# Kernel tuning notes

Measured on AMD Instinct MI355X. Metric: run time of the kernel, lower is better.

Reference implementation:

```python
import jax, jax.numpy as jnp
import numpy as np

NB_OBJ = 5
DIM_BODY = 10
DIM_OBJ = 15
N_PERM = NB_OBJ * (NB_OBJ - 1)  # 20
LOG_STD_MIN, LOG_STD_MAX = -20.0, 2.0


def _linear_init(key, fan_in, fan_out):
    k1, k2 = jax.random.split(key)
    lim = 1.0 / np.sqrt(fan_in)
    W = jax.random.uniform(k1, (fan_in, fan_out), minval=-lim, maxval=lim, dtype=jnp.float32)
    b = jax.random.uniform(k2, (fan_out,), minval=-lim, maxval=lim, dtype=jnp.float32)
    return W, b


def setup_inputs() -> dict:
    key = jax.random.key(0)
    ks = jax.random.split(key, 12)
    B = 16384
    # graph structure (constants)
    perms = [(i, j) for i in range(NB_OBJ) for j in range(NB_OBJ) if i != j]
    src = jnp.array([p[0] for p in perms], dtype=jnp.int32)   # [E]
    dst = jnp.array([p[1] for p in perms], dtype=jnp.int32)   # [E]
    inc = jnp.array([[k for k, p in enumerate(perms) if p[1] == i] for i in range(NB_OBJ)], dtype=jnp.int32)  # [O,4]
    pred = jnp.arange(2 * N_PERM, dtype=jnp.int32).reshape(N_PERM, 2)  # predicate ids per edge
    # parameters
    mp_W1, mp_b1 = _linear_init(ks[0], 8, 256)
    mp_W2, mp_b2 = _linear_init(ks[1], 256, 128)
    ea_W, ea_b = _linear_init(ks[2], 128, 1)
    phi_W1, phi_b1 = _linear_init(ks[3], 153, 256)
    phi_W2, phi_b2 = _linear_init(ks[4], 256, 128)
    sa_W, sa_b = _linear_init(ks[5], 128, 1)
    rho_W1, rho_b1 = _linear_init(ks[6], 128, 256)
    mean_W, mean_b = _linear_init(ks[7], 256, 4)
    ls_W, ls_b = _linear_init(ks[8], 256, 4)
    obs = jax.random.normal(ks[9], (B, DIM_BODY + NB_OBJ * DIM_OBJ), dtype=jnp.float32)
    ag = jax.random.normal(ks[10], (B, 2 * N_PERM), dtype=jnp.float32)
    g = jax.random.normal(ks[11], (B, 2 * N_PERM), dtype=jnp.float32)
    return dict(obs=obs, ag=ag, g=g,
                mp_W1=mp_W1, mp_b1=mp_b1, mp_W2=mp_W2, mp_b2=mp_b2,
                ea_W=ea_W, ea_b=ea_b,
                phi_W1=phi_W1, phi_b1=phi_b1, phi_W2=phi_W2, phi_b2=phi_b2,
                sa_W=sa_W, sa_b=sa_b,
                rho_W1=rho_W1, rho_b1=rho_b1,
                mean_W=mean_W, mean_b=mean_b, ls_W=ls_W, ls_b=ls_b,
                src=src, dst=dst, inc=inc, pred=pred)


def reference(obs, ag, g,
              mp_W1, mp_b1, mp_W2, mp_b2,
              ea_W, ea_b,
              phi_W1, phi_b1, phi_W2, phi_b2,
              sa_W, sa_b,
              rho_W1, rho_b1,
              mean_W, mean_b, ls_W, ls_b,
              src, dst, inc, pred):
    B = obs.shape[0]
    body = obs[:, :DIM_BODY]                                    # [B,10]
    objs = obs[:, DIM_BODY:].reshape(B, NB_OBJ, DIM_OBJ)        # [B,O,15]
    delta_g = g - ag                                            # [B,40]
    # --- message passing over edges (vectorized gather + cat) ---
    e_pred = delta_g[:, pred]                                   # [B,E,2]
    e_src = objs[:, src, :3]                                    # [B,E,3]
    e_dst = objs[:, dst, :3]                                    # [B,E,3]
    inp_mp = jnp.concatenate([e_pred, e_src, e_dst], axis=-1)   # [B,E,8]
    h = jax.nn.relu(inp_mp @ mp_W1 + mp_b1)
    mp_out = jax.nn.relu(h @ mp_W2 + mp_b2)                     # [B,E,128]
    # --- edge self-attention pooling per object over incoming edges ---
    per_obj = mp_out[:, inc]                                    # [B,O,K,128]
    w = jax.nn.softmax(per_obj @ ea_W + ea_b, axis=2)           # softmax over incoming set
    edge_feat = jnp.sum(w * per_obj, axis=2)                    # [B,O,128]
    # --- deep-set phi over objects ---
    body_rep = jnp.broadcast_to(body[:, None, :], (B, NB_OBJ, DIM_BODY))
    inp = jnp.concatenate([body_rep, objs, edge_feat], axis=-1)  # [B,O,153]
    ph = jax.nn.relu(inp @ phi_W1 + phi_b1)
    phi_out = jax.nn.relu(ph @ phi_W2 + phi_b2)                  # [B,O,128]
    aw = jax.nn.softmax(phi_out @ sa_W + sa_b, axis=1)           # softmax over objects
    pooled = jnp.sum(aw * phi_out, axis=1)                       # [B,128]
    # --- rho actor head ---
    r = jax.nn.relu(pooled @ rho_W1 + rho_b1)
    mean = r @ mean_W + mean_b
    logstd = jnp.clip(r @ ls_W + ls_b, LOG_STD_MIN, LOG_STD_MAX)
    return mean, logstd
```

## Files before the change

kernel.cpp:

```cpp
#include <hip/hip_runtime.h>
#include <cstdint>
#include <cstddef>

typedef unsigned short u16;
typedef unsigned int u32;
typedef __attribute__((ext_vector_type(8))) short bf16x8;
typedef __attribute__((ext_vector_type(4))) float f32x4;

#define MFMA16(A, B, C) __builtin_amdgcn_mfma_f32_16x16x32_bf16((A), (B), (C), 0, 0, 0)

__device__ __forceinline__ u16 bf16_rne(float x) {
    u32 u = __float_as_uint(x);
    u += 0x7fffu + ((u >> 16) & 1u);
    return (u16)(u >> 16);
}
__device__ __forceinline__ float bf2f(u16 h) { return __uint_as_float((u32)h << 16); }
__device__ __forceinline__ u16 bf16_lo(float x, u16 hi) { return bf16_rne(x - bf2f(hi)); }
__device__ __forceinline__ float blo(u32 u) { return __uint_as_float(u << 16); }
__device__ __forceinline__ float bhi(u32 u) { return __uint_as_float(u & 0xffff0000u); }
__device__ __forceinline__ u32 cvt_pk(float a, float b) {
    u32 r;
    asm("v_cvt_pk_bf16_f32 %0, %1, %2" : "=v"(r) : "v"(a), "v"(b));
    return r;
}

__device__ __forceinline__ void PK_body(int tid,
    const float* __restrict__ mpW1, const float* __restrict__ mpW2,
    const float* __restrict__ phW1, const float* __restrict__ phW2,
    const float* __restrict__ rhoW,
    u16* __restrict__ Bp1e, u16* __restrict__ Bp2e,
    u16* __restrict__ BpC1, u16* __restrict__ BpC2, u16* __restrict__ BpR)
{
    if (tid < 8192) {
        int t = tid >> 9, r = tid & 511;
        int l = r >> 3, i = r & 7, g = l >> 4, l15 = l & 15;
        float w = mpW1[i * 256 + 16 * t + l15];
        u16 h = bf16_rne(w);
        Bp1e[tid] = (g < 2) ? h : bf16_lo(w, h);
    } else if (tid < 73728) {
        int f = tid - 8192;
        int b5 = f >> 9, r = f & 511;
        int l = r >> 3, i = r & 7, g = l >> 4, l15 = l & 15;
        int s = b5 & 1, cn = b5 >> 1, c = cn >> 3, n = cn & 7;
        int kk = 32 * c + 8 * g + i;
        float w = mpW2[kk * 128 + 16 * n + l15];
        u16 h = bf16_rne(w);
        Bp2e[f] = s ? bf16_lo(w, h) : h;
    } else if (tid < 155648) {
        int f = tid - 73728;
        int b5 = f >> 9, r = f & 511;
        int l = r >> 3, i = r & 7, g = l >> 4, l15 = l & 15;
        int t = b5 & 15, cs = b5 >> 4, s = cs & 1, c = cs >> 1;
        int kk = 32 * c + 8 * g + i;
        int kp = kk < 25 ? kk : (kk < 32 ? -1 : kk - 7);
        float w = (kp < 0) ? 0.0f : phW1[kp * 256 + 16 * t + l15];
        u16 h = bf16_rne(w);
        BpC1[f] = s ? bf16_lo(w, h) : h;
    } else if (tid < 221184) {
        int f = tid - 155648;
        int b5 = f >> 9, r = f & 511;
        int l = r >> 3, i = r & 7, g = l >> 4, l15 = l & 15;
        int s = b5 & 1, cn = b5 >> 1, c = cn >> 3, n = cn & 7;
        int kk = 32 * c + 8 * g + i;
        float w = phW2[kk * 128 + 16 * n + l15];
        u16 h = bf16_rne(w);
        BpC2[f] = s ? bf16_lo(w, h) : h;
    } else {
        int f = tid - 221184;
        int b5 = f >> 9, r = f & 511;
        int l = r >> 3, i = r & 7, g = l >> 4, l15 = l & 15;
        int s = b5 & 1, ct = b5 >> 1, c = ct >> 4, t = ct & 15;
        int kk = 32 * c + 8 * g + i;
        float w = rhoW[kk * 256 + 16 * t + l15];
        u16 h = bf16_rne(w);
        BpR[f] = s ? bf16_lo(w, h) : h;
    }
}

__device__ __forceinline__ void P1_body(int row,
    const float* __restrict__ obs, const float* __restrict__ ag, const float* __restrict__ g,
    const int* __restrict__ src, const int* __restrict__ dst, const int* __restrict__ pred,
    u16* __restrict__ Ein)
{
    int b = row / 20, p = row - b * 20;
    float inp[8];
    int i0 = pred[2 * p], i1 = pred[2 * p + 1];
    const float* gb = g + (size_t)b * 40;
    const float* ab = ag + (size_t)b * 40;
    inp[0] = gb[i0] - ab[i0];
    inp[1] = gb[i1] - ab[i1];
    int so = src[p], dd = dst[p];
    const float* ob = obs + (size_t)b * 85 + 10;
    inp[2] = ob[so * 15 + 0]; inp[3] = ob[so * 15 + 1]; inp[4] = ob[so * 15 + 2];
    inp[5] = ob[dd * 15 + 0]; inp[6] = ob[dd * 15 + 1]; inp[7] = ob[dd * 15 + 2];

    u32 wh[4], wl[4];
    #pragma unroll
    for (int k = 0; k < 4; ++k) {
        u16 h0 = bf16_rne(inp[2 * k]), h1 = bf16_rne(inp[2 * k + 1]);
        u16 l0 = bf16_lo(inp[2 * k], h0), l1 = bf16_lo(inp[2 * k + 1], h1);
        wh[k] = (u32)h0 | ((u32)h1 << 16);
        wl[k] = (u32)l0 | ((u32)l1 << 16);
    }
    uint4* d4 = (uint4*)(Ein + (size_t)row * 16);
    d4[0] = make_uint4(wh[0], wh[1], wh[2], wh[3]);
    d4[1] = make_uint4(wl[0], wl[1], wl[2], wl[3]);
}

__global__ __launch_bounds__(256) void PREP(
    const float* __restrict__ mpW1, const float* __restrict__ mpW2,
    const float* __restrict__ phW1, const float* __restrict__ phW2,
    const float* __restrict__ rhoW,
    u16* __restrict__ Bp1e, u16* __restrict__ Bp2e,
    u16* __restrict__ BpC1, u16* __restrict__ BpC2, u16* __restrict__ BpR,
    const float* __restrict__ obs, const float* __restrict__ ag, const float* __restrict__ g,
    const int* __restrict__ src, const int* __restrict__ dst, const int* __restrict__ pred,
    u16* __restrict__ Ein,
    const float* __restrict__ meanW, const float* __restrict__ lsW,
    float* __restrict__ headWpk)
{
    int bid = blockIdx.x;
    if (bid < 1120) {
        PK_body(bid * 256 + threadIdx.x, mpW1, mpW2, phW1, phW2, rhoW, Bp1e, Bp2e, BpC1, BpC2, BpR);
    } else if (bid < 2400) {
        P1_body((bid - 1120) * 256 + threadIdx.x, obs, ag, g, src, dst, pred, Ein);
    } else {
        int idx = threadIdx.x;
        #pragma unroll
        for (int r = 0; r < 8; ++r) {
            int f = r * 256 + idx;
            int k = f >> 3, q = f & 7;
            headWpk[f] = (q < 4) ? meanW[k * 4 + q] : lsW[k * 4 + (q - 4)];
        }
    }
}

__global__ __launch_bounds__(512) void GA(
    const u16* __restrict__ Ein, const u16* __restrict__ Bp1, const u16* __restrict__ Bp2,
    const float* __restrict__ b1, const float* __restrict__ b2,
    const float* __restrict__ eaW, const float* __restrict__ eab,
    const int* __restrict__ inc, const float* __restrict__ obs,
    u16* __restrict__ Nin)
{
    __shared__ u16 hb[3][16 * 256];
    __shared__ u16 mpb[80 * 128];
    __shared__ float spart[8][80];
    __shared__ float wbuf[80];
    __shared__ int rowb[80];
    __shared__ int incL[20];

    const int tid = threadIdx.x;
    const int w = tid >> 6, lane = tid & 63;
    const int l15 = lane & 15, gq = lane >> 4;
    const int rowbase = blockIdx.x * 80;
    char* hbc = (char*)hb;
    char* mpc = (char*)mpb;

    if (tid < 20) incL[tid] = inc[tid];

    bf16x8 B1[2];
    float4 b1v[2];
    #pragma unroll
    for (int t = 0; t < 2; ++t) {
        B1[t] = *(const bf16x8*)(Bp1 + (size_t)(2 * w + t) * 512 + lane * 8);
        b1v[t] = *(const float4*)(b1 + 16 * (2 * w + t) + 4 * gq);
    }
    bf16x8 B2[8];
    #pragma unroll
    for (int c = 0; c < 8; ++c)
        B2[c] = *(const bf16x8*)(Bp2 + (size_t)((c * 8 + w) * 2) * 512 + lane * 8);
    const float4 b2v = *(const float4*)(b2 + 16 * w + 4 * gq);
    const float4 eav = *(const float4*)(eaW + 16 * w + 4 * gq);

    auto ldX = [&](int m) {
        return *(const bf16x8*)(Ein + (size_t)(rowbase + m * 16 + l15) * 16 + 8 * (gq & 1));
    };
    auto stage1 = [&](int buf, const bf16x8& X) {
        #pragma unroll
        for (int t = 0; t < 2; ++t) {
            f32x4 acc = {b1v[t].x, b1v[t].y, b1v[t].z, b1v[t].w};
            acc = MFMA16(B1[t], X, acc);
            u32 p0 = cvt_pk(fmaxf(acc[0], 0.f), fmaxf(acc[1], 0.f));
            u32 p1 = cvt_pk(fmaxf(acc[2], 0.f), fmaxf(acc[3], 0.f));
            int colu = 16 * (2 * w + t) + 4 * gq;
            int byte = buf * 8192 + ((l15 * 512 + colu * 2) ^ ((l15 & 7) << 4));
            *(uint2*)(hbc + byte) = make_uint2(p0, p1);
        }
    };
    auto stage2 = [&](int m, int buf) {
        f32x4 accA = {b2v.x, b2v.y, b2v.z, b2v.w};
        f32x4 accB = {0.f, 0.f, 0.f, 0.f};
        #pragma unroll
        for (int c = 0; c < 4; ++c) {
            int byteA = buf * 8192 + ((l15 * 512 + (2 * c) * 64 + gq * 16) ^ ((l15 & 7) << 4));
            int byteB = buf * 8192 + ((l15 * 512 + (2 * c + 1) * 64 + gq * 16) ^ ((l15 & 7) << 4));
            const bf16x8 HA = *(const bf16x8*)(hbc + byteA);
            const bf16x8 HB = *(const bf16x8*)(hbc + byteB);
            accA = MFMA16(B2[2 * c], HA, accA);
            accB = MFMA16(B2[2 * c + 1], HB, accB);
        }
        float v0 = fmaxf(accA[0] + accB[0], 0.f), v1 = fmaxf(accA[1] + accB[1], 0.f);
        float v2 = fmaxf(accA[2] + accB[2], 0.f), v3 = fmaxf(accA[3] + accB[3], 0.f);
        float ep = v0 * eav.x + v1 * eav.y + v2 * eav.z + v3 * eav.w;
        ep += __shfl_xor(ep, 16, 64);
        ep += __shfl_xor(ep, 32, 64);
        if (gq == 0) spart[w][m * 16 + l15] = ep;
        u32 p0 = cvt_pk(v0, v1), p1 = cvt_pk(v2, v3);
        int r = m * 16 + l15;
        int byte2 = (r * 256 + (16 * w + 4 * gq) * 2) ^ ((r & 15) << 4);
        *(uint2*)(mpc + byte2) = make_uint2(p0, p1);
    };

    {
        bf16x8 X0 = ldX(0);
        bf16x8 X1 = ldX(1);
        stage1(0, X0);
        stage1(1, X1);
    }
    __syncthreads();
    {
        bf16x8 X2 = ldX(2);
        stage2(0, 0);
        stage2(1, 1);
        stage1(2, X2);
    }
    __syncthreads();
    {
        bf16x8 X3 = ldX(3);
        bf16x8 X4 = ldX(4);
        stage2(2, 2);
        stage1(0, X3);
        stage1(1, X4);
    }
    __syncthreads();
    stage2(3, 0);
    stage2(4, 1);
    __syncthreads();

    if (tid < 20) {
        int bl = tid / 5, o = tid - bl * 5;
        const float e0 = eab[0];
        int rr[4]; float ee[4];
        #pragma unroll
        for (int i = 0; i < 4; ++i) {
            rr[i] = bl * 20 + incL[o * 4 + i];
            float e = e0;
            #pragma unroll
            for (int ww = 0; ww < 8; ++ww) e += spart[ww][rr[i]];
            ee[i] = e;
        }
        float mx = fmaxf(fmaxf(ee[0], ee[1]), fmaxf(ee[2], ee[3]));
        float ex[4]; float den = 0.f;
        #pragma unroll
        for (int i = 0; i < 4; ++i) { ex[i] = __expf(ee[i] - mx); den += ex[i]; }
        float inv = 1.0f / den;
        #pragma unroll
        for (int i = 0; i < 4; ++i) {
            wbuf[tid * 4 + i] = ex[i] * inv;
            rowb[tid * 4 + i] = rr[i];
        }
    } else if (tid >= 320 && tid < 480) {
        int t2 = tid - 320;
        int p = t2 >> 3, q = t2 & 7;
        int bl = p / 5, o = p - bl * 5;
        const float* body = obs + (size_t)(blockIdx.x * 4 + bl) * 85;
        const float* op = body + 10 + o * 15;
        float v[4];
        #pragma unroll
        for (int jj = 0; jj < 4; ++jj) {
            int col = 4 * q + jj;
            v[jj] = (col < 10) ? body[col] : (col < 25) ? op[col - 10] : 0.0f;
        }
        int grow = blockIdx.x * 20 + p;
        *(uint2*)(Nin + (size_t)grow * 160 + 4 * q) =
            make_uint2(cvt_pk(v[0], v[1]), cvt_pk(v[2], v[3]));
    }
    __syncthreads();

    if (tid < 320) {
        int p = tid >> 4, cb = tid & 15;
        float acc[8] = {0, 0, 0, 0, 0, 0, 0, 0};
        #pragma unroll
        for (int i = 0; i < 4; ++i) {
            int r = rowb[p * 4 + i];
            float wi = wbuf[p * 4 + i];
            int byte = (r * 256 + cb * 16) ^ ((r & 15) << 4);
            uint4 v = *(const uint4*)(mpc + byte);
            acc[0] = fmaf(wi, blo(v.x), acc[0]);
            acc[1] = fmaf(wi, bhi(v.x), acc[1]);
            acc[2] = fmaf(wi, blo(v.y), acc[2]);
            acc[3] = fmaf(wi, bhi(v.y), acc[3]);
            acc[4] = fmaf(wi, blo(v.z), acc[4]);
            acc[5] = fmaf(wi, bhi(v.z), acc[5]);
            acc[6] = fmaf(wi, blo(v.w), acc[6]);
            acc[7] = fmaf(wi, bhi(v.w), acc[7]);
        }
        uint4 ov;
        ov.x = cvt_pk(acc[0], acc[1]);
        ov.y = cvt_pk(acc[2], acc[3]);
        ov.z = cvt_pk(acc[4], acc[5]);
        ov.w = cvt_pk(acc[6], acc[7]);
        int grow = blockIdx.x * 20 + p;
        *(uint4*)(Nin + (size_t)grow * 160 + 32 + cb * 8) = ov;
    }
}

__global__ __launch_bounds__(512) void GB(
    const u16* __restrict__ Nin, const u16* __restrict__ BpC1, const u16* __restrict__ BpC2,
    const u16* __restrict__ BpR,
    const float* __restrict__ b1, const float* __restrict__ b2,
    const float* __restrict__ saW, const float* __restrict__ sab,
    const float* __restrict__ rhob, const float* __restrict__ headWpk,
    const float* __restrict__ meanb, const float* __restrict__ lsb,
    float* __restrict__ outp)
{
    __shared__ u16 hb[4][16 * 256];
    __shared__ u16 phibuf[80 * 132];
    __shared__ float spart[8][80];
    __shared__ float awb[80];

    const int tid = threadIdx.x;
    const int w = tid >> 6, lane = tid & 63;
    const int l15 = lane & 15, gq = lane >> 4;
    const int rowbase = blockIdx.x * 80;
    char* hbc = (char*)hb;
    float* rbuf = (float*)phibuf;
    float* hpart = (float*)spart;
    u32* poolw = (u32*)hb;

    bf16x8 BC[5][2];
    float4 b1v[2];
    #pragma unroll
    for (int t = 0; t < 2; ++t) b1v[t] = *(const float4*)(b1 + 16 * (2 * w + t) + 4 * gq);
    #pragma unroll
    for (int c = 0; c < 5; ++c)
        #pragma unroll
        for (int t = 0; t < 2; ++t)
            BC[c][t] = *(const bf16x8*)(BpC1 + (size_t)((c * 2) * 16 + 2 * w + t) * 512 + lane * 8);
    bf16x8 B2[8];
    #pragma unroll
    for (int c = 0; c < 8; ++c)
        B2[c] = *(const bf16x8*)(BpC2 + (size_t)((c * 8 + w) * 2) * 512 + lane * 8);
    const float4 b2v = *(const float4*)(b2 + 16 * w + 4 * gq);
    const float4 sav = *(const float4*)(saW + 16 * w + 4 * gq);

    auto loadX = [&](int m, bf16x8* X) {
        #pragma unroll
        for (int c = 0; c < 5; ++c)
            X[c] = *(const bf16x8*)(Nin + (size_t)(rowbase + m * 16 + l15) * 160 + 32 * c + 8 * gq);
    };
    auto stage1 = [&](int buf, const bf16x8* X) {
        f32x4 a0 = {b1v[0].x, b1v[0].y, b1v[0].z, b1v[0].w};
        f32x4 a1 = {b1v[1].x, b1v[1].y, b1v[1].z, b1v[1].w};
        #pragma unroll
        for (int c = 0; c < 5; ++c) {
            a0 = MFMA16(BC[c][0], X[c], a0);
            a1 = MFMA16(BC[c][1], X[c], a1);
        }
        #pragma unroll
        for (int t = 0; t < 2; ++t) {
            const f32x4& a = t ? a1 : a0;
            u32 p0 = cvt_pk(fmaxf(a[0], 0.f), fmaxf(a[1], 0.f));
            u32 p1 = cvt_pk(fmaxf(a[2], 0.f), fmaxf(a[3], 0.f));
            int colu = 16 * (2 * w + t) + 4 * gq;
            int byte = buf * 8192 + ((l15 * 512 + colu * 2) ^ ((l15 & 7) << 4));
            *(uint2*)(hbc + byte) = make_uint2(p0, p1);
        }
    };
    auto stage2 = [&](int m, int buf) {
        f32x4 accA = {b2v.x, b2v.y, b2v.z, b2v.w};
        f32x4 accB = {0.f, 0.f, 0.f, 0.f};
        #pragma unroll
        for (int c = 0; c < 4; ++c) {
            int byteA = buf * 8192 + ((l15 * 512 + (2 * c) * 64 + gq * 16) ^ ((l15 & 7) << 4));
            int byteB = buf * 8192 + ((l15 * 512 + (2 * c + 1) * 64 + gq * 16) ^ ((l15 & 7) << 4));
            const bf16x8 HA = *(const bf16x8*)(hbc + byteA);
            const bf16x8 HB = *(const bf16x8*)(hbc + byteB);
            accA = MFMA16(B2[2 * c], HA, accA);
            accB = MFMA16(B2[2 * c + 1], HB, accB);
        }
        float v0 = fmaxf(accA[0] + accB[0], 0.f), v1 = fmaxf(accA[1] + accB[1], 0.f);
        float v2 = fmaxf(accA[2] + accB[2], 0.f), v3 = fmaxf(accA[3] + accB[3], 0.f);
        int r = m * 16 + l15;
        *(uint2*)((char*)phibuf + r * 264 + (16 * w + 4 * gq) * 2) =
            make_uint2(cvt_pk(v0, v1), cvt_pk(v2, v3));
        float sp = v0 * sav.x + v1 * sav.y + v2 * sav.z + v3 * sav.w;
        sp += __shfl_xor(sp, 16, 64);
        sp += __shfl_xor(sp, 32, 64);
        if (gq == 0) spart[w][r] = sp;
    };

    {
        bf16x8 X0[5], X1[5];
        loadX(0, X0);
        loadX(1, X1);
        stage1(0, X0);
        stage1(1, X1);
    }
    __syncthreads();
    {
        bf16x8 X2[5], X3[5];
        loadX(2, X2);
        loadX(3, X3);
        stage2(0, 0);
        stage2(1, 1);
        stage1(2, X2);
        stage1(3, X3);
    }
    __syncthreads();
    {
        bf16x8 X4[5];
        loadX(4, X4);
        stage2(2, 2);
        stage2(3, 3);
        stage1(0, X4);
    }
    __syncthreads();
    stage2(4, 0);
    __syncthreads();

    if (tid < 16) {
        const float s0c = sab[0];
        float ss[5];
        #pragma unroll
        for (int o = 0; o < 5; ++o) {
            float s = s0c;
            #pragma unroll
            for (int ww = 0; ww < 8; ++ww) s += spart[ww][tid * 5 + o];
            ss[o] = s;
        }
        float mx = fmaxf(fmaxf(fmaxf(ss[0], ss[1]), fmaxf(ss[2], ss[3])), ss[4]);
        float ex[5]; float den = 0.f;
        #pragma unroll
        for (int o = 0; o < 5; ++o) { ex[o] = __expf(ss[o] - mx); den += ex[o]; }
        float inv = 1.0f / den;
        #pragma unroll
        for (int o = 0; o < 5; ++o) awb[tid * 5 + o] = ex[o] * inv;
    }
    __syncthreads();

    #pragma unroll
    for (int rep = 0; rep < 2; ++rep) {
        int idx = rep * 512 + tid;
        int b = idx >> 6, cw = idx & 63;
        float p0 = 0.f, p1 = 0.f;
        #pragma unroll
        for (int o = 0; o < 5; ++o) {
            u32 v = *(const u32*)((const char*)phibuf + (size_t)(b * 5 + o) * 264 + cw * 4);
            float a = awb[b * 5 + o];
            p0 = fmaf(a, blo(v), p0);
            p1 = fmaf(a, bhi(v), p1);
        }
        u16 h0 = bf16_rne(p0); u16 l0 = bf16_lo(p0, h0);
        u16 h1 = bf16_rne(p1); u16 l1 = bf16_lo(p1, h1);
        *(uint2*)(poolw + b * 132 + 2 * cw) =
            make_uint2((u32)h0 | ((u32)l0 << 16), (u32)h1 | ((u32)l1 << 16));
    }
    __syncthreads();

    {
        float4 rb0 = *(const float4*)(rhob + 16 * (2 * w + 0) + 4 * gq);
        float4 rb1 = *(const float4*)(rhob + 16 * (2 * w + 1) + 4 * gq);
        f32x4 acc0 = {rb0.x, rb0.y, rb0.z, rb0.w};
        f32x4 acc1 = {rb1.x, rb1.y, rb1.z, rb1.w};
        #pragma unroll
        for (int c = 0; c < 4; ++c) {
            uint4 q0 = *(const uint4*)(poolw + l15 * 132 + 32 * c + 8 * gq);
            uint4 q1 = *(const uint4*)(poolw + l15 * 132 + 32 * c + 8 * gq + 4);
            u32 ws[8] = {q0.x, q0.y, q0.z, q0.w, q1.x, q1.y, q1.z, q1.w};
            bf16x8 Ph, Pl;
            #pragma unroll
            for (int i = 0; i < 8; ++i) {
                Ph[i] = (short)(ws[i] & 0xffffu);
                Pl[i] = (short)(ws[i] >> 16);
            }
            #pragma unroll
            for (int t = 0; t < 2; ++t) {
                bf16x8 Bh = *(const bf16x8*)(BpR + (size_t)((c * 16 + 2 * w + t) * 2 + 0) * 512 + lane * 8);
                f32x4& a = t ? acc1 : acc0;
                a = MFMA16(Bh, Ph, a);
                a = MFMA16(Bh, Pl, a);
            }
        }
        #pragma unroll
        for (int t = 0; t < 2; ++t) {
            const f32x4& a = t ? acc1 : acc0;
            float4 v;
            v.x = fmaxf(a[0], 0.f); v.y = fmaxf(a[1], 0.f);
            v.z = fmaxf(a[2], 0.f); v.w = fmaxf(a[3], 0.f);
            *(float4*)(rbuf + l15 * 260 + 16 * (2 * w + t) + 4 * gq) = v;
        }
    }
    __syncthreads();

    {
        int s = tid >> 7, p = tid & 127;
        int b = p >> 3, q = p & 7;
        const float* rrow = rbuf + b * 260 + s * 64;
        const float* wcol = headWpk + s * 64 * 8 + q;
        float acc = 0.f;
        #pragma unroll 8
        for (int k = 0; k < 64; ++k)
            acc = fmaf(rrow[k], wcol[k * 8], acc);
        hpart[s * 128 + p] = acc;
    }
    __syncthreads();
    if (tid < 128) {
        int b = tid >> 3, q = tid & 7;
        float a = hpart[tid] + hpart[128 + tid] + hpart[256 + tid] + hpart[384 + tid];
        int bg = blockIdx.x * 16 + b;
        if (q < 4) {
            outp[(size_t)bg * 4 + q] = a + meanb[q];
        } else {
            float l = a + lsb[q - 4];
            outp[65536 + (size_t)bg * 4 + (q - 4)] = fminf(fmaxf(l, -20.0f), 2.0f);
        }
    }
}

extern "C" void kernel_launch(void* const* d_in, const int* in_sizes, int n_in,
                              void* d_out, int out_size, void* d_ws, size_t ws_size,
                              hipStream_t stream)
{
    const float* obs   = (const float*)d_in[0];
    const float* ag    = (const float*)d_in[1];
    const float* g     = (const float*)d_in[2];
    const float* mpW1  = (const float*)d_in[3];
    const float* mpb1  = (const float*)d_in[4];
    const float* mpW2  = (const float*)d_in[5];
    const float* mpb2  = (const float*)d_in[6];
    const float* eaW   = (const float*)d_in[7];
    const float* eab   = (const float*)d_in[8];
    const float* phW1  = (const float*)d_in[9];
    const float* phb1  = (const float*)d_in[10];
    const float* phW2  = (const float*)d_in[11];
    const float* phb2  = (const float*)d_in[12];
    const float* saW   = (const float*)d_in[13];
    const float* sab   = (const float*)d_in[14];
    const float* rhoW  = (const float*)d_in[15];
    const float* rhob  = (const float*)d_in[16];
    const float* meanW = (const float*)d_in[17];
    const float* meanb = (const float*)d_in[18];
    const float* lsW   = (const float*)d_in[19];
    const float* lsb   = (const float*)d_in[20];
    const int*   src   = (const int*)d_in[21];
    const int*   dst   = (const int*)d_in[22];
    const int*   inc   = (const int*)d_in[23];
    const int*   pred  = (const int*)d_in[24];

    char* ws = (char*)d_ws;
    u16* Ein  = (u16*)(ws + 0);
    u16* Nin  = (u16*)(ws + 10485760ull);
    u16* Bp1e = (u16*)(ws + 36700160ull);
    u16* Bp2e = (u16*)(ws + 36716544ull);
    u16* BpC1 = (u16*)(ws + 36847616ull);
    u16* BpC2 = (u16*)(ws + 37011456ull);
    u16* BpR  = (u16*)(ws + 37142528ull);
    float* headWpk = (float*)(ws + 37273600ull);

    hipLaunchKernelGGL(PREP, dim3(2401), dim3(256), 0, stream,
                       mpW1, mpW2, phW1, phW2, rhoW, Bp1e, Bp2e, BpC1, BpC2, BpR,
                       obs, ag, g, src, dst, pred, Ein, meanW, lsW, headWpk);
    hipLaunchKernelGGL(GA, dim3(4096), dim3(512), 0, stream,
                       Ein, Bp1e, Bp2e, mpb1, mpb2, eaW, eab, inc, obs, Nin);
    hipLaunchKernelGGL(GB, dim3(1024), dim3(512), 0, stream,
                       Nin, BpC1, BpC2, BpR, phb1, phb2, saW, sab, rhob,
                       headWpk, meanb, lsb, (float*)d_out);
}
```

Baseline: 98.45 us.

## Fuse edge and node kernels into one kernel, keeping node inputs in LDS

Merges the edge message-passing kernel (GA) and the node/deep-set kernel (GB) into a single kernel GF with 1024 blocks. Each block loops over four 80-edge groups to build its 80 node input rows directly in shared memory, so the Nin global buffer round trip and one launch go away. In exchange the grid is 4x smaller, and the larger LDS footprint (~76KB) and heavier per-block work may reduce occupancy and latency hiding.

Result: slower. 105.3 us (+6.9%).

```diff
diff --git a/kernel.cpp b/kernel.cpp
--- a/kernel.cpp
+++ b/kernel.cpp
@@ -135,385 +135,378 @@
     }
 }
 
-__global__ __launch_bounds__(512) void GA(
+__global__ __launch_bounds__(512) void GF(
     const u16* __restrict__ Ein, const u16* __restrict__ Bp1, const u16* __restrict__ Bp2,
-    const float* __restrict__ b1, const float* __restrict__ b2,
+    const float* __restrict__ eb1, const float* __restrict__ eb2,
     const float* __restrict__ eaW, const float* __restrict__ eab,
     const int* __restrict__ inc, const float* __restrict__ obs,
-    u16* __restrict__ Nin)
-{
-    __shared__ u16 hb[3][16 * 256];
-    __shared__ u16 mpb[80 * 128];
-    __shared__ float spart[8][80];
-    __shared__ float wbuf[80];
-    __shared__ int rowb[80];
-    __shared__ int incL[20];
-
-    const int tid = threadIdx.x;
-    const int w = tid >> 6, lane = tid & 63;
-    const int l15 = lane & 15, gq = lane >> 4;
-    const int rowbase = blockIdx.x * 80;
-    char* hbc = (char*)hb;
-    char* mpc = (char*)mpb;
-
-    if (tid < 20) incL[tid] = inc[tid];
-
-    bf16x8 B1[2];
-    float4 b1v[2];
-    #pragma unroll
-    for (int t = 0; t < 2; ++t) {
-        B1[t] = *(const bf16x8*)(Bp1 + (size_t)(2 * w + t) * 512 + lane * 8);
-        b1v[t] = *(const float4*)(b1 + 16 * (2 * w + t) + 4 * gq);
-    }
-    bf16x8 B2[8];
-    #pragma unroll
-    for (int c = 0; c < 8; ++c)
-        B2[c] = *(const bf16x8*)(Bp2 + (size_t)((c * 8 + w) * 2) * 512 + lane * 8);
-    const float4 b2v = *(const float4*)(b2 + 16 * w + 4 * gq);
-    const float4 eav = *(const float4*)(eaW + 16 * w + 4 * gq);
-
-    auto ldX = [&](int m) {
-        return *(const bf16x8*)(Ein + (size_t)(rowbase + m * 16 + l15) * 16 + 8 * (gq & 1));
-    };
-    auto stage1 = [&](int buf, const bf16x8& X) {
-        #pragma unroll
-        for (int t = 0; t < 2; ++t) {
-            f32x4 acc = {b1v[t].x, b1v[t].y, b1v[t].z, b1v[t].w};
-            acc = MFMA16(B1[t], X, acc);
-            u32 p0 = cvt_pk(fmaxf(acc[0], 0.f), fmaxf(acc[1], 0.f));
-            u32 p1 = cvt_pk(fmaxf(acc[2], 0.f), fmaxf(acc[3], 0.f));
-            int colu = 16 * (2 * w + t) + 4 * gq;
-            int byte = buf * 8192 + ((l15 * 512 + colu * 2) ^ ((l15 & 7) << 4));
-            *(uint2*)(hbc + byte) = make_uint2(p0, p1);
-        }
-    };
-    auto stage2 = [&](int m, int buf) {
-        f32x4 accA = {b2v.x, b2v.y, b2v.z, b2v.w};
-        f32x4 accB = {0.f, 0.f, 0.f, 0.f};
-        #pragma unroll
-        for (int c = 0; c < 4; ++c) {
-            int byteA = buf * 8192 + ((l15 * 512 + (2 * c) * 64 + gq * 16) ^ ((l15 & 7) << 4));
-            int byteB = buf * 8192 + ((l15 * 512 + (2 * c + 1) * 64 + gq * 16) ^ ((l15 & 7) << 4));
-            const bf16x8 HA = *(const bf16x8*)(hbc + byteA);
-            const bf16x8 HB = *(const bf16x8*)(hbc + byteB);
-            accA = MFMA16(B2[2 * c], HA, accA);
-            accB = MFMA16(B2[2 * c + 1], HB, accB);
-        }
-        float v0 = fmaxf(accA[0] + accB[0], 0.f), v1 = fmaxf(accA[1] + accB[1], 0.f);
-        float v2 = fmaxf(accA[2] + accB[2], 0.f), v3 = fmaxf(accA[3] + accB[3], 0.f);
-        float ep = v0 * eav.x + v1 * eav.y + v2 * eav.z + v3 * eav.w;
-        ep += __shfl_xor(ep, 16, 64);
-        ep += __shfl_xor(ep, 32, 64);
-        if (gq == 0) spart[w][m * 16 + l15] = ep;
-        u32 p0 = cvt_pk(v0, v1), p1 = cvt_pk(v2, v3);
-        int r = m * 16 + l15;
-        int byte2 = (r * 256 + (16 * w + 4 * gq) * 2) ^ ((r & 15) << 4);
-        *(uint2*)(mpc + byte2) = make_uint2(p0, p1);
-    };
-
-    {
-        bf16x8 X0 = ldX(0);
-        bf16x8 X1 = ldX(1);
-        stage1(0, X0);
-        stage1(1, X1);
-    }
-    __syncthreads();
-    {
-        bf16x8 X2 = ldX(2);
-        stage2(0, 0);
-        stage2(1, 1);
-        stage1(2, X2);
-    }
-    __syncthreads();
-    {
-        bf16x8 X3 = ldX(3);
-        bf16x8 X4 = ldX(4);
-        stage2(2, 2);
-        stage1(0, X3);
-        stage1(1, X4);
-    }
-    __syncthreads();
-    stage2(3, 0);
-    stage2(4, 1);
-    __syncthreads();
-
-    if (tid < 20) {
-        int bl = tid / 5, o = tid - bl * 5;
-        const float e0 = eab[0];
-        int rr[4]; float ee[4];
-        #pragma unroll
-        for (int i = 0; i < 4; ++i) {
-            rr[i] = bl * 20 + incL[o * 4 + i];
-            float e = e0;
-            #pragma unroll
-            for (int ww = 0; ww < 8; ++ww) e += spart[ww][rr[i]];
-            ee[i] = e;
-        }
-        float mx = fmaxf(fmaxf(ee[0], ee[1]), fmaxf(ee[2], ee[3]));
-        float ex[4]; float den = 0.f;
-        #pragma unroll
-        for (int i = 0; i < 4; ++i) { ex[i] = __expf(ee[i] - mx); den += ex[i]; }
-        float inv = 1.0f / den;
-        #pragma unroll
-        for (int i = 0; i < 4; ++i) {
-            wbuf[tid * 4 + i] = ex[i] * inv;
-            rowb[tid * 4 + i] = rr[i];
-        }
-    } else if (tid >= 320 && tid < 480) {
-        int t2 = tid - 320;
-        int p = t2 >> 3, q = t2 & 7;
-        int bl = p / 5, o = p - bl * 5;
-        const float* body = obs + (size_t)(blockIdx.x * 4 + bl) * 85;
-        const float* op = body + 10 + o * 15;
-        float v[4];
-        #pragma unroll
-        for (int jj = 0; jj < 4; ++jj) {
-            int col = 4 * q + jj;
-            v[jj] = (col < 10) ? body[col] : (col < 25) ? op[col - 10] : 0.0f;
-        }
-        int grow = blockIdx.x * 20 + p;
-        *(uint2*)(Nin + (size_t)grow * 160 + 4 * q) =
-            make_uint2(cvt_pk(v[0], v[1]), cvt_pk(v[2], v[3]));
-    }
-    __syncthreads();
-
-    if (tid < 320) {
-        int p = tid >> 4, cb = tid & 15;
-        float acc[8] = {0, 0, 0, 0, 0, 0, 0, 0};
-        #pragma unroll
-        for (int i = 0; i < 4; ++i) {
-            int r = rowb[p * 4 + i];
-            float wi = wbuf[p * 4 + i];
-            int byte = (r * 256 + cb * 16) ^ ((r & 15) << 4);
-            uint4 v = *(const uint4*)(mpc + byte);
-            acc[0] = fmaf(wi, blo(v.x), acc[0]);
-            acc[1] = fmaf(wi, bhi(v.x), acc[1]);
-            acc[2] = fmaf(wi, blo(v.y), acc[2]);
-            acc[3] = fmaf(wi, bhi(v.y), acc[3]);
-            acc[4] = fmaf(wi, blo(v.z), acc[4]);
-            acc[5] = fmaf(wi, bhi(v.z), acc[5]);
-            acc[6] = fmaf(wi, blo(v.w), acc[6]);
-            acc[7] = fmaf(wi, bhi(v.w), acc[7]);
-        }
-        uint4 ov;
-        ov.x = cvt_pk(acc[0], acc[1]);
-        ov.y = cvt_pk(acc[2], acc[3]);
-        ov.z = cvt_pk(acc[4], acc[5]);
-        ov.w = cvt_pk(acc[6], acc[7]);
-        int grow = blockIdx.x * 20 + p;
-        *(uint4*)(Nin + (size_t)grow * 160 + 32 + cb * 8) = ov;
-    }
-}
-
-__global__ __launch_bounds__(512) void GB(
-    const u16* __restrict__ Nin, const u16* __restrict__ BpC1, const u16* __restrict__ BpC2,
-    const u16* __restrict__ BpR,
-    const float* __restrict__ b1, const float* __restrict__ b2,
+    const u16* __restrict__ BpC1, const u16* __restrict__ BpC2, const u16* __restrict__ BpR,
+    const float* __restrict__ nb1, const float* __restrict__ nb2,
     const float* __restrict__ saW, const float* __restrict__ sab,
     const float* __restrict__ rhob, const float* __restrict__ headWpk,
     const float* __restrict__ meanb, const float* __restrict__ lsb,
     float* __restrict__ outp)
 {
-    __shared__ u16 hb[4][16 * 256];
-    __shared__ u16 phibuf[80 * 132];
-    __shared__ float spart[8][80];
-    __shared__ float awb[80];
-
+    __shared__ __align__(16) char S[76176];
     const int tid = threadIdx.x;
     const int w = tid >> 6, lane = tid & 63;
     const int l15 = lane & 15, gq = lane >> 4;
-    const int rowbase = blockIdx.x * 80;
-    char* hbc = (char*)hb;
-    float* rbuf = (float*)phibuf;
-    float* hpart = (float*)spart;
-    u32* poolw = (u32*)hb;
-
-    bf16x8 BC[5][2];
-    float4 b1v[2];
-    #pragma unroll
-    for (int t = 0; t < 2; ++t) b1v[t] = *(const float4*)(b1 + 16 * (2 * w + t) + 4 * gq);
-    #pragma unroll
-    for (int c = 0; c < 5; ++c)
-        #pragma unroll
-        for (int t = 0; t < 2; ++t)
-            BC[c][t] = *(const bf16x8*)(BpC1 + (size_t)((c * 2) * 16 + 2 * w + t) * 512 + lane * 8);
-    bf16x8 B2[8];
-    #pragma unroll
-    for (int c = 0; c < 8; ++c)
-        B2[c] = *(const bf16x8*)(BpC2 + (size_t)((c * 8 + w) * 2) * 512 + lane * 8);
-    const float4 b2v = *(const float4*)(b2 + 16 * w + 4 * gq);
-    const float4 sav = *(const float4*)(saW + 16 * w + 4 * gq);
-
-    auto loadX = [&](int m, bf16x8* X) {
+    char* hbc = S;
+    char* mpc = S + 24576;
+    char* ninc = S + 45696;
+    float* spart = (float*)(S + 72576);
+    float* wbuf = (float*)(S + 75136);
+    float* awb  = (float*)(S + 75456);
+    int*   rowb = (int*)(S + 75776);
+    int*   incL = (int*)(S + 76096);
+
+    if (tid < 20) incL[tid] = inc[tid];
+
+    {
+        bf16x8 B1[2];
+        float4 b1v[2];
+        #pragma unroll
+        for (int t = 0; t < 2; ++t) {
+            B1[t] = *(const bf16x8*)(Bp1 + (size_t)(2 * w + t) * 512 + lane * 8);
+            b1v[t] = *(const float4*)(eb1 + 16 * (2 * w + t) + 4 * gq);
+        }
+        bf16x8 B2[8];
+        #pragma unroll
+        for (int c = 0; c < 8; ++c)
+            B2[c] = *(const bf16x8*)(Bp2 + (size_t)((c * 8 + w) * 2) * 512 + lane * 8);
+        const float4 b2v = *(const float4*)(eb2 + 16 * w + 4 * gq);
+        const float4 eav = *(const float4*)(eaW + 16 * w + 4 * gq);
+
+        auto stage1e = [&](int buf, const bf16x8& X) {
+            #pragma unroll
+            for (int t = 0; t < 2; ++t) {
+                f32x4 acc = {b1v[t].x, b1v[t].y, b1v[t].z, b1v[t].w};
+                acc = MFMA16(B1[t], X, acc);
+                u32 p0 = cvt_pk(fmaxf(acc[0], 0.f), fmaxf(acc[1], 0.f));
+                u32 p1 = cvt_pk(fmaxf(acc[2], 0.f), fmaxf(acc[3], 0.f));
+                int colu = 16 * (2 * w + t) + 4 * gq;
+                int byte = buf * 8192 + ((l15 * 512 + colu * 2) ^ ((l15 & 7) << 4));
+                *(uint2*)(hbc + byte) = make_uint2(p0, p1);
+            }
+        };
+        auto stage2e = [&](int m, int buf) {
+            f32x4 accA = {b2v.x, b2v.y, b2v.z, b2v.w};
+            f32x4 accB = {0.f, 0.f, 0.f, 0.f};
+            #pragma unroll
+            for (int c = 0; c < 4; ++c) {
+                int byteA = buf * 8192 + ((l15 * 512 + (2 * c) * 64 + gq * 16) ^ ((l15 & 7) << 4));
+                int byteB = buf * 8192 + ((l15 * 512 + (2 * c + 1) * 64 + gq * 16) ^ ((l15 & 7) << 4));
+                const bf16x8 HA = *(const bf16x8*)(hbc + byteA);
+                const bf16x8 HB = *(const bf16x8*)(hbc + byteB);
+                accA = MFMA16(B2[2 * c], HA, accA);
+                accB = MFMA16(B2[2 * c + 1], HB, accB);
+            }
+            float v0 = fmaxf(accA[0] + accB[0], 0.f), v1 = fmaxf(accA[1] + accB[1], 0.f);
+            float v2 = fmaxf(accA[2] + accB[2], 0.f), v3 = fmaxf(accA[3] + accB[3], 0.f);
+            float ep = v0 * eav.x + v1 * eav.y + v2 * eav.z + v3 * eav.w;
+            ep += __shfl_xor(ep, 16, 64);
+            ep += __shfl_xor(ep, 32, 64);
+            if (gq == 0) spart[w * 80 + m * 16 + l15] = ep;
+            u32 p0 = cvt_pk(v0, v1), p1 = cvt_pk(v2, v3);
+            int r = m * 16 + l15;
+            int byte2 = (r * 256 + (16 * w + 4 * gq) * 2) ^ ((r & 15) << 4);
+            *(uint2*)(mpc + byte2) = make_uint2(p0, p1);
+        };
+
+        #pragma unroll 1
+        for (int g = 0; g < 4; ++g) {
+            const int rowbaseE = blockIdx.x * 320 + g * 80;
+            auto ldX = [&](int m) {
+                return *(const bf16x8*)(Ein + (size_t)(rowbaseE + m * 16 + l15) * 16 + 8 * (gq & 1));
+            };
+            {
+                bf16x8 X0 = ldX(0);
+                bf16x8 X1 = ldX(1);
+                stage1e(0, X0);
+                stage1e(1, X1);
+            }
+            __syncthreads();
+            {
+                bf16x8 X2 = ldX(2);
+                stage2e(0, 0);
+                stage2e(1, 1);
+                stage1e(2, X2);
+            }
+            __syncthreads();
+            {
+                bf16x8 X3 = ldX(3);
+                bf16x8 X4 = ldX(4);
+                stage2e(2, 2);
+                stage1e(0, X3);
+                stage1e(1, X4);
+            }
+            __syncthreads();
+            stage2e(3, 0);
+            stage2e(4, 1);
+            __syncthreads();
+
+            if (tid < 20) {
+                int bl = tid / 5, o = tid - bl * 5;
+                const float e0 = eab[0];
+                int rr[4]; float ee[4];
+                #pragma unroll
+                for (int i = 0; i < 4; ++i) {
+                    rr[i] = bl * 20 + incL[o * 4 + i];
+                    float e = e0;
+                    #pragma unroll
+                    for (int ww = 0; ww < 8; ++ww) e += spart[ww * 80 + rr[i]];
+                    ee[i] = e;
+                }
+                float mx = fmaxf(fmaxf(ee[0], ee[1]), fmaxf(ee[2], ee[3]));
+                float ex[4]; float den = 0.f;
+                #pragma unroll
+                for (int i = 0; i < 4; ++i) { ex[i] = __expf(ee[i] - mx); den += ex[i]; }
+                float inv = 1.0f / den;
+                #pragma unroll
+                for (int i = 0; i < 4; ++i) {
+                    wbuf[tid * 4 + i] = ex[i] * inv;
+                    rowb[tid * 4 + i] = rr[i];
+                }
+            } else if (tid >= 320 && tid < 480) {
+                int t2 = tid - 320;
+                int p = t2 >> 3, q = t2 & 7;
+                int bl = p / 5, o = p - bl * 5;
+                const float* body = obs + (size_t)(blockIdx.x * 16 + g * 4 + bl) * 85;
+                const float* op = body + 10 + o * 15;
+                float v[4];
+                #pragma unroll
+                for (int jj = 0; jj < 4; ++jj) {
+                    int col = 4 * q + jj;
+                    v[jj] = (col < 10) ? body[col] : (col < 25) ? op[col - 10] : 0.0f;
+                }
+                *(uint2*)(ninc + (size_t)(g * 20 + p) * 336 + q * 8) =
+                    make_uint2(cvt_pk(v[0], v[1]), cvt_pk(v[2], v[3]));
+            }
+            __syncthreads();
+
+            if (tid < 320) {
+                int p = tid >> 4, cb = tid & 15;
+                float acc[8] = {0, 0, 0, 0, 0, 0, 0, 0};
+                #pragma unroll
+                for (int i = 0; i < 4; ++i) {
+                    int r = rowb[p * 4 + i];
+                    float wi = wbuf[p * 4 + i];
+                    int byte = (r * 256 + cb * 16) ^ ((r & 15) << 4);
+                    uint4 v = *(const uint4*)(mpc + byte);
+                    acc[0] = fmaf(wi, blo(v.x), acc[0]);
+                    acc[1] = fmaf(wi, bhi(v.x), acc[1]);
+                    acc[2] = fmaf(wi, blo(v.y), acc[2]);
+                    acc[3] = fmaf(wi, bhi(v.y), acc[3]);
+                    acc[4] = fmaf(wi, blo(v.z), acc[4]);
+                    acc[5] = fmaf(wi, bhi(v.z), acc[5]);
+                    acc[6] = fmaf(wi, blo(v.w), acc[6]);
+                    acc[7] = fmaf(wi, bhi(v.w), acc[7]);
+                }
+                uint4 ov;
+                ov.x = cvt_pk(acc[0], acc[1]);
+                ov.y = cvt_pk(acc[2], acc[3]);
+                ov.z = cvt_pk(acc[4], acc[5]);
+                ov.w = cvt_pk(acc[6], acc[7]);
+                *(uint4*)(ninc + (size_t)(g * 20 + p) * 336 + 64 + cb * 16) = ov;
+            }
+            __syncthreads();
+        }
+    }
+
+    __builtin_amdgcn_sched_barrier(0);
+
+    {
+        float* rbuf = (float*)mpc;
+        float* hpart = spart;
+        u32* poolw = (u32*)hbc;
+
+        bf16x8 BC[5][2];
+        float4 b1v[2];
+        #pragma unroll
+        for (int t = 0; t < 2; ++t) b1v[t] = *(const float4*)(nb1 + 16 * (2 * w + t) + 4 * gq);
         #pragma unroll
         for (int c = 0; c < 5; ++c)
-            X[c] = *(const bf16x8*)(Nin + (size_t)(rowbase + m * 16 + l15) * 160 + 32 * c + 8 * gq);
-    };
-    auto stage1 = [&](int buf, const bf16x8* X) {
-        f32x4 a0 = {b1v[0].x, b1v[0].y, b1v[0].z, b1v[0].w};
-        f32x4 a1 = {b1v[1].x, b1v[1].y, b1v[1].z, b1v[1].w};
-        #pragma unroll
-        for (int c = 0; c < 5; ++c) {
-            a0 = MFMA16(BC[c][0], X[c], a0);
-            a1 = MFMA16(BC[c][1], X[c], a1);
-        }
-        #pragma unroll
-        for (int t = 0; t < 2; ++t) {
-            const f32x4& a = t ? a1 : a0;
-            u32 p0 = cvt_pk(fmaxf(a[0], 0.f), fmaxf(a[1], 0.f));
-            u32 p1 = cvt_pk(fmaxf(a[2], 0.f), fmaxf(a[3], 0.f));
-            int colu = 16 * (2 * w + t) + 4 * gq;
-            int byte = buf * 8192 + ((l15 * 512 + colu * 2) ^ ((l15 & 7) << 4));
-            *(uint2*)(hbc + byte) = make_uint2(p0, p1);
-        }
-    };
-    auto stage2 = [&](int m, int buf) {
-        f32x4 accA = {b2v.x, b2v.y, b2v.z, b2v.w};
-        f32x4 accB = {0.f, 0.f, 0.f, 0.f};
-        #pragma unroll
-        for (int c = 0; c < 4; ++c) {
-            int byteA = buf * 8192 + ((l15 * 512 + (2 * c) * 64 + gq * 16) ^ ((l15 & 7) << 4));
-            int byteB = buf * 8192 + ((l15 * 512 + (2 * c + 1) * 64 + gq * 16) ^ ((l15 & 7) << 4));
-            const bf16x8 HA = *(const bf16x8*)(hbc + byteA);
-            const bf16x8 HB = *(const bf16x8*)(hbc + byteB);
-            accA = MFMA16(B2[2 * c], HA, accA);
-            accB = MFMA16(B2[2 * c + 1], HB, accB);
-        }
-        float v0 = fmaxf(accA[0] + accB[0], 0.f), v1 = fmaxf(accA[1] + accB[1], 0.f);
-        float v2 = fmaxf(accA[2] + accB[2], 0.f), v3 = fmaxf(accA[3] + accB[3], 0.f);
-        int r = m * 16 + l15;
-        *(uint2*)((char*)phibuf + r * 264 + (16 * w + 4 * gq) * 2) =
-            make_uint2(cvt_pk(v0, v1), cvt_pk(v2, v3));
-        float sp = v0 * sav.x + v1 * sav.y + v2 * sav.z + v3 * sav.w;
-        sp += __shfl_xor(sp, 16, 64);
-        sp += __shfl_xor(sp, 32, 64);
-        if (gq == 0) spart[w][r] = sp;
-    };
-
-    {
-        bf16x8 X0[5], X1[5];
-        loadX(0, X0);
-        loadX(1, X1);
-        stage1(0, X0);
-        stage1(1, X1);
-    }
-    __syncthreads();
-    {
-        bf16x8 X2[5], X3[5];
-        loadX(2, X2);
-        loadX(3, X3);
-        stage2(0, 0);
-        stage2(1, 1);
-        stage1(2, X2);
-        stage1(3, X3);
-    }
-    __syncthreads();
-    {
-        bf16x8 X4[5];
-        loadX(4, X4);
-        stage2(2, 2);
-        stage2(3, 3);
-        stage1(0, X4);
-    }
-    __syncthreads();
-    stage2(4, 0);
-    __syncthreads();
-
-    if (tid < 16) {
-        const float s0c = sab[0];
-        float ss[5];
-        #pragma unroll
-        for (int o = 0; o < 5; ++o) {
-            float s = s0c;
-            #pragma unroll
-            for (int ww = 0; ww < 8; ++ww) s += spart[ww][tid * 5 + o];
-            ss[o] = s;
-        }
-        float mx = fmaxf(fmaxf(fmaxf(ss[0], ss[1]), fmaxf(ss[2], ss[3])), ss[4]);
-        float ex[5]; float den = 0.f;
-        #pragma unroll
-        for (int o = 0; o < 5; ++o) { ex[o] = __expf(ss[o] - mx); den += ex[o]; }
-        float inv = 1.0f / den;
-        #pragma unroll
-        for (int o = 0; o < 5; ++o) awb[tid * 5 + o] = ex[o] * inv;
-    }
-    __syncthreads();
-
-    #pragma unroll
-    for (int rep = 0; rep < 2; ++rep) {
-        int idx = rep * 512 + tid;
-        int b = idx >> 6, cw = idx & 63;
-        float p0 = 0.f, p1 = 0.f;
-        #pragma unroll
-        for (int o = 0; o < 5; ++o) {
-            u32 v = *(const u32*)((const char*)phibuf + (size_t)(b * 5 + o) * 264 + cw * 4);
-            float a = awb[b * 5 + o];
-            p0 = fmaf(a, blo(v), p0);
-            p1 = fmaf(a, bhi(v), p1);
-        }
-        u16 h0 = bf16_rne(p0); u16 l0 = bf16_lo(p0, h0);
-        u16 h1 = bf16_rne(p1); u16 l1 = bf16_lo(p1, h1);
-        *(uint2*)(poolw + b * 132 + 2 * cw) =
-            make_uint2((u32)h0 | ((u32)l0 << 16), (u32)h1 | ((u32)l1 << 16));
-    }
-    __syncthreads();
-
-    {
-        float4 rb0 = *(const float4*)(rhob + 16 * (2 * w + 0) + 4 * gq);
-        float4 rb1 = *(const float4*)(rhob + 16 * (2 * w + 1) + 4 * gq);
-        f32x4 acc0 = {rb0.x, rb0.y, rb0.z, rb0.w};
-        f32x4 acc1 = {rb1.x, rb1.y, rb1.z, rb1.w};
-        #pragma unroll
-        for (int c = 0; c < 4; ++c) {
-            uint4 q0 = *(const uint4*)(poolw + l15 * 132 + 32 * c + 8 * gq);
-            uint4 q1 = *(const uint4*)(poolw + l15 * 132 + 32 * c + 8 * gq + 4);
-            u32 ws[8] = {q0.x, q0.y, q0.z, q0.w, q1.x, q1.y, q1.z, q1.w};
-            bf16x8 Ph, Pl;
-            #pragma unroll
-            for (int i = 0; i < 8; ++i) {
-                Ph[i] = (short)(ws[i] & 0xffffu);
-                Pl[i] = (short)(ws[i] >> 16);
+            #pragma unroll
+            for (int t = 0; t < 2; ++t)
+                BC[c][t] = *(const bf16x8*)(BpC1 + (size_t)((c * 2) * 16 + 2 * w + t) * 512 + lane * 8);
+        bf16x8 B2[8];
+        #pragma unroll
+        for (int c = 0; c < 8; ++c)
+            B2[c] = *(const bf16x8*)(BpC2 + (size_t)((c * 8 + w) * 2) * 512 + lane * 8);
+        const float4 b2v = *(const float4*)(nb2 + 16 * w + 4 * gq);
+        const float4 sav = *(const float4*)(saW + 16 * w + 4 * gq);
+
+        auto loadX = [&](int m, bf16x8* X) {
+            #pragma unroll
+            for (int c = 0; c < 5; ++c)
+                X[c] = *(const bf16x8*)(ninc + (size_t)(m * 16 + l15) * 336 + c * 64 + gq * 16);
+        };
+        auto stage1n = [&](int buf, const bf16x8* X) {
+            f32x4 a0 = {b1v[0].x, b1v[0].y, b1v[0].z, b1v[0].w};
+            f32x4 a1 = {b1v[1].x, b1v[1].y, b1v[1].z, b1v[1].w};
+            #pragma unroll
+            for (int c = 0; c < 5; ++c) {
+                a0 = MFMA16(BC[c][0], X[c], a0);
+                a1 = MFMA16(BC[c][1], X[c], a1);
             }
             #pragma unroll
             for (int t = 0; t < 2; ++t) {
-                bf16x8 Bh = *(const bf16x8*)(BpR + (size_t)((c * 16 + 2 * w + t) * 2 + 0) * 512 + lane * 8);
-                f32x4& a = t ? acc1 : acc0;
-                a = MFMA16(Bh, Ph, a);
-                a = MFMA16(Bh, Pl, a);
-            }
-        }
-        #pragma unroll
-        for (int t = 0; t < 2; ++t) {
-            const f32x4& a = t ? acc1 : acc0;
-            float4 v;
-            v.x = fmaxf(a[0], 0.f); v.y = fmaxf(a[1], 0.f);
-            v.z = fmaxf(a[2], 0.f); v.w = fmaxf(a[3], 0.f);
-            *(float4*)(rbuf + l15 * 260 + 16 * (2 * w + t) + 4 * gq) = v;
-        }
-    }
-    __syncthreads();
-
-    {
-        int s = tid >> 7, p = tid & 127;
-        int b = p >> 3, q = p & 7;
-        const float* rrow = rbuf + b * 260 + s * 64;
-        const float* wcol = headWpk + s * 64 * 8 + q;
-        float acc = 0.f;
-        #pragma unroll 8
-        for (int k = 0; k < 64; ++k)
-            acc = fmaf(rrow[k], wcol[k * 8], acc);
-        hpart[s * 128 + p] = acc;
-    }
-    __syncthreads();
-    if (tid < 128) {
-        int b = tid >> 3, q = tid & 7;
-        float a = hpart[tid] + hpart[128 + tid] + hpart[256 + tid] + hpart[384 + tid];
-        int bg = blockIdx.x * 16 + b;
-        if (q < 4) {
-            outp[(size_t)bg * 4 + q] = a + meanb[q];
-        } else {
-            float l = a + lsb[q - 4];
-            outp[65536 + (size_t)bg * 4 + (q - 4)] = fminf(fmaxf(l, -20.0f), 2.0f);
+                const f32x4& a = t ? a1 : a0;
+                u32 p0 = cvt_pk(fmaxf(a[0], 0.f), fmaxf(a[1], 0.f));
+                u32 p1 = cvt_pk(fmaxf(a[2], 0.f), fmaxf(a[3], 0.f));
+                int colu = 16 * (2 * w + t) + 4 * gq;
+                int byte = buf * 8192 + ((l15 * 512 + colu * 2) ^ ((l15 & 7) << 4));
+                *(uint2*)(hbc + byte) = make_uint2(p0, p1);
+            }
+        };
+        auto stage2n = [&](int m, int buf) {
+            f32x4 accA = {b2v.x, b2v.y, b2v.z, b2v.w};
+            f32x4 accB = {0.f, 0.f, 0.f, 0.f};
+            #pragma unroll
+            for (int c = 0; c < 4; ++c) {
+                int byteA = buf * 8192 + ((l15 * 512 + (2 * c) * 64 + gq * 16) ^ ((l15 & 7) << 4));
+                int byteB = buf * 8192 + ((l15 * 512 + (2 * c + 1) * 64 + gq * 16) ^ ((l15 & 7) << 4));
+                const bf16x8 HA = *(const bf16x8*)(hbc + byteA);
+                const bf16x8 HB = *(const bf16x8*)(hbc + byteB);
+                accA = MFMA16(B2[2 * c], HA, accA);
+                accB = MFMA16(B2[2 * c + 1], HB, accB);
+            }
+            float v0 = fmaxf(accA[0] + accB[0], 0.f), v1 = fmaxf(accA[1] + accB[1], 0.f);
+            float v2 = fmaxf(accA[2] + accB[2], 0.f), v3 = fmaxf(accA[3] + accB[3], 0.f);
+            int r = m * 16 + l15;
+            *(uint2*)(mpc + r * 264 + (16 * w + 4 * gq) * 2) =
+                make_uint2(cvt_pk(v0, v1), cvt_pk(v2, v3));
+            float sp = v0 * sav.x + v1 * sav.y + v2 * sav.z + v3 * sav.w;
+            sp += __shfl_xor(sp, 16, 64);
+            sp += __shfl_xor(sp, 32, 64);
+            if (gq == 0) spart[w * 80 + r] = sp;
+        };
+
+        {
+            bf16x8 X0[5], X1[5];
+            loadX(0, X0);
+            loadX(1, X1);
+            stage1n(0, X0);
+            stage1n(1, X1);
+        }
+        __syncthreads();
+        {
+            bf16x8 X2[5];
+            loadX(2, X2);
+            stage2n(0, 0);
+            stage2n(1, 1);
+            stage1n(2, X2);
+        }
+        __syncthreads();
+        {
+            bf16x8 X3[5], X4[5];
+            loadX(3, X3);
+            loadX(4, X4);
+            stage2n(2, 2);
+            stage1n(0, X3);
+            stage1n(1, X4);
+        }
+        __syncthreads();
+        stage2n(3, 0);
+        stage2n(4, 1);
+        __syncthreads();
+
+        if (tid < 16) {
+            const float s0c = sab[0];
+            float ss[5];
+            #pragma unroll
+            for (int o = 0; o < 5; ++o) {
+                float s = s0c;
+                #pragma unroll
+                for (int ww = 0; ww < 8; ++ww) s += spart[ww * 80 + tid * 5 + o];
+                ss[o] = s;
+            }
+            float mx = fmaxf(fmaxf(fmaxf(ss[0], ss[1]), fmaxf(ss[2], ss[3])), ss[4]);
+            float ex[5]; float den = 0.f;
+            #pragma unroll
+            for (int o = 0; o < 5; ++o) { ex[o] = __expf(ss[o] - mx); den += ex[o]; }
+            float inv = 1.0f / den;
+            #pragma unroll
+            for (int o = 0; o < 5; ++o) awb[tid * 5 + o] = ex[o] * inv;
+        }
+        __syncthreads();
+
+        #pragma unroll
+        for (int rep = 0; rep < 2; ++rep) {
+            int idx = rep * 512 + tid;
+            int b = idx >> 6, cw = idx & 63;
+            float p0 = 0.f, p1 = 0.f;
+            #pragma unroll
+            for (int o = 0; o < 5; ++o) {
+                u32 v = *(const u32*)(mpc + (size_t)(b * 5 + o) * 264 + cw * 4);
+                float a = awb[b * 5 + o];
+                p0 = fmaf(a, blo(v), p0);
+                p1 = fmaf(a, bhi(v), p1);
+            }
+            u16 h0 = bf16_rne(p0); u16 l0 = bf16_lo(p0, h0);
+            u16 h1 = bf16_rne(p1); u16 l1 = bf16_lo(p1, h1);
+            *(uint2*)(poolw + b * 132 + 2 * cw) =
+                make_uint2((u32)h0 | ((u32)l0 << 16), (u32)h1 | ((u32)l1 << 16));
+        }
+        __syncthreads();
+
+        {
+            float4 rb0 = *(const float4*)(rhob + 16 * (2 * w + 0) + 4 * gq);
+            float4 rb1 = *(const float4*)(rhob + 16 * (2 * w + 1) + 4 * gq);
+            f32x4 acc0 = {rb0.x, rb0.y, rb0.z, rb0.w};
+            f32x4 acc1 = {rb1.x, rb1.y, rb1.z, rb1.w};
+            #pragma unroll
+            for (int c = 0; c < 4; ++c) {
+                uint4 q0 = *(const uint4*)(poolw + l15 * 132 + 32 * c + 8 * gq);
+                uint4 q1 = *(const uint4*)(poolw + l15 * 132 + 32 * c + 8 * gq + 4);
+                u32 ws[8] = {q0.x, q0.y, q0.z, q0.w, q1.x, q1.y, q1.z, q1.w};
+                bf16x8 Ph, Pl;
+                #pragma unroll
+                for (int i = 0; i < 8; ++i) {
+                    Ph[i] = (short)(ws[i] & 0xffffu);
+                    Pl[i] = (short)(ws[i] >> 16);
+                }
+                #pragma unroll
+                for (int t = 0; t < 2; ++t) {
+                    bf16x8 Bh = *(const bf16x8*)(BpR + (size_t)((c * 16 + 2 * w + t) * 2 + 0) * 512 + lane * 8);
+                    f32x4& a = t ? acc1 : acc0;
+                    a = MFMA16(Bh, Ph, a);
+                    a = MFMA16(Bh, Pl, a);
+                }
+            }
+            #pragma unroll
+            for (int t = 0; t < 2; ++t) {
+                const f32x4& a = t ? acc1 : acc0;
+                float4 v;
+                v.x = fmaxf(a[0], 0.f); v.y = fmaxf(a[1], 0.f);
+                v.z = fmaxf(a[2], 0.f); v.w = fmaxf(a[3], 0.f);
+                *(float4*)(rbuf + l15 * 260 + 16 * (2 * w + t) + 4 * gq) = v;
+            }
+        }
+        __syncthreads();
+
+        {
+            int s = tid >> 7, p = tid & 127;
+            int b = p >> 3, q = p & 7;
+            const float* rrow = rbuf + b * 260 + s * 64;
+            const float* wcol = headWpk + s * 64 * 8 + q;
+            float acc = 0.f;
+            #pragma unroll 8
+            for (int k = 0; k < 64; ++k)
+                acc = fmaf(rrow[k], wcol[k * 8], acc);
+            hpart[s * 128 + p] = acc;
+        }
+        __syncthreads();
+        if (tid < 128) {
+            int b = tid >> 3, q = tid & 7;
+            float a = hpart[tid] + hpart[128 + tid] + hpart[256 + tid] + hpart[384 + tid];
+            int bg = blockIdx.x * 16 + b;
+            if (q < 4) {
+                outp[(size_t)bg * 4 + q] = a + meanb[q];
+            } else {
+                float l = a + lsb[q - 4];
+                outp[65536 + (size_t)bg * 4 + (q - 4)] = fminf(fmaxf(l, -20.0f), 2.0f);
+            }
         }
     }
 }
@@ -550,7 +543,6 @@
 
     char* ws = (char*)d_ws;
     u16* Ein  = (u16*)(ws + 0);
-    u16* Nin  = (u16*)(ws + 10485760ull);
     u16* Bp1e = (u16*)(ws + 36700160ull);
     u16* Bp2e = (u16*)(ws + 36716544ull);
     u16* BpC1 = (u16*)(ws + 36847616ull);
@@ -561,9 +553,8 @@
     hipLaunchKernelGGL(PREP, dim3(2401), dim3(256), 0, stream,
                        mpW1, mpW2, phW1, phW2, rhoW, Bp1e, Bp2e, BpC1, BpC2, BpR,
                        obs, ag, g, src, dst, pred, Ein, meanW, lsW, headWpk);
-    hipLaunchKernelGGL(GA, dim3(4096), dim3(512), 0, stream,
-                       Ein, Bp1e, Bp2e, mpb1, mpb2, eaW, eab, inc, obs, Nin);
-    hipLaunchKernelGGL(GB, dim3(1024), dim3(512), 0, stream,
-                       Nin, BpC1, BpC2, BpR, phb1, phb2, saW, sab, rhob,
+    hipLaunchKernelGGL(GF, dim3(1024), dim3(512), 0, stream,
+                       Ein, Bp1e, Bp2e, mpb1, mpb2, eaW, eab, inc, obs,
+                       BpC1, BpC2, BpR, phb1, phb2, saW, sab, rhob,
                        headWpk, meanb, lsb, (float*)d_out);
 }
```
